# Optimization experiments

Hardware: AMD Instinct MI355X
Metric: run time of the kernel (lower is better)

## Reference

```python
import jax, jax.numpy as jnp
import numpy as np

B, T, H, ZS, ZT = 256, 512, 256, 64, 64
N_IRR = 2
TAU = 1.0
EPS = 1e-5

def setup_inputs() -> dict:
    key = jax.random.key(0)
    ks = jax.random.split(key, 32)
    def p(k, shape):
        return jax.random.normal(k, shape, jnp.float32) * 0.05
    gru_in_dim = ZT + H + 1 + N_IRR * 2  # 325
    return {
        "z_static": jax.random.normal(ks[0], (B, ZS), jnp.float32),
        "z_temporal": jax.random.normal(ks[1], (B, T, ZT), jnp.float32),
        "initial_states": jax.random.uniform(ks[2], (B, N_IRR, 2), jnp.float32),
        "sn_w1": p(ks[3], (H, ZS)), "sn_b1": p(ks[4], (H,)),
        "bn1_g": jnp.ones((H,), jnp.float32), "bn1_b": jnp.zeros((H,), jnp.float32),
        "sn_w2": p(ks[5], (H, H)), "sn_b2": p(ks[6], (H,)),
        "bn2_g": jnp.ones((H,), jnp.float32), "bn2_b": jnp.zeros((H,), jnp.float32),
        "sc_w": p(ks[7], (8, H)), "sc_b": p(ks[8], (8,)),
        "scat1_w": p(ks[9], (4, H)), "scat1_b": p(ks[10], (4,)),
        "scat2_w": p(ks[11], (6, H)), "scat2_b": p(ks[12], (6,)),
        "gru_wih": p(ks[13], (3 * H, gru_in_dim)), "gru_whh": p(ks[14], (3 * H, H)),
        "gru_bih": p(ks[15], (3 * H,)), "gru_bhh": p(ks[16], (3 * H,)),
        "tc_w": p(ks[17], (16, H)), "tc_b": p(ks[18], (16,)),
        "irr1_w": p(ks[19], (1, H)), "irr1_b": p(ks[20], (1,)),
        "irr2_w": p(ks[21], (1, H)), "irr2_b": p(ks[22], (1,)),
        "tcat_w": p(ks[23], (5, H)), "tcat_b": p(ks[24], (5,)),
    }

def _bn(x, g, b):
    # BatchNorm1d in training mode: batch stats, biased variance
    m = jnp.mean(x, axis=0)
    v = jnp.mean((x - m) ** 2, axis=0)
    return (x - m) * jax.lax.rsqrt(v + EPS) * g + b

def _gumbel_softmax(logits, k):
    g = jax.random.gumbel(k, logits.shape, logits.dtype)
    return jax.nn.softmax((logits + g) / TAU, axis=-1)

def _gru(x_proj, whh, bhh):
    # x_proj: [B,T,3H] = x @ Wih^T + bih, precomputed (big GEMM once)
    h0 = jnp.zeros((x_proj.shape[0], H), x_proj.dtype)
    def step(h, xp):
        gh = h @ whh.T + bhh
        xr, xz, xn = jnp.split(xp, 3, axis=-1)
        hr, hz, hn = jnp.split(gh, 3, axis=-1)
        r = jax.nn.sigmoid(xr + hr)
        z = jax.nn.sigmoid(xz + hz)
        n = jnp.tanh(xn + r * hn)
        h_new = (1.0 - z) * n + z * h
        return h_new, h_new
    _, hs = jax.lax.scan(step, h0, jnp.swapaxes(x_proj, 0, 1))  # [T,B,H]
    return jnp.swapaxes(hs, 0, 1)  # [B,T,H]

def _forward(z_static, z_temporal, initial_states, sn_w1, sn_b1, bn1_g, bn1_b,
             sn_w2, sn_b2, bn2_g, bn2_b, sc_w, sc_b, scat1_w, scat1_b,
             scat2_w, scat2_b, gru_wih, gru_whh, gru_bih, gru_bhh,
             tc_w, tc_b, irr1_w, irr1_b, irr2_w, irr2_b, tcat_w, tcat_b):
    b, t = z_temporal.shape[0], z_temporal.shape[1]
    baseline = _bn(jax.nn.relu(z_static @ sn_w1.T + sn_b1), bn1_g, bn1_b)
    baseline = _bn(jax.nn.relu(baseline @ sn_w2.T + sn_b2), bn2_g, bn2_b)  # [B,H]

    static_cont = jnp.tanh(baseline @ sc_w.T + sc_b) * 0.5 + 0.5  # [B,8]
    gk = jax.random.split(jax.random.key(42), 3)
    static_cat = jnp.concatenate([
        _gumbel_softmax(baseline @ scat1_w.T + scat1_b, gk[0]),
        _gumbel_softmax(baseline @ scat2_w.T + scat2_b, gk[1]),
    ], axis=-1)  # [B,10]

    baseline_exp = jnp.broadcast_to(baseline[:, None, :], (b, t, H))
    visit = jnp.broadcast_to(jnp.linspace(0.0, 1.0, t, dtype=z_temporal.dtype)[None, :, None], (b, t, 1))
    init = jnp.broadcast_to(initial_states.reshape(b, 1, N_IRR * 2), (b, t, N_IRR * 2))
    gru_in = jnp.concatenate([z_temporal, baseline_exp, visit, init], axis=-1)  # [B,T,325]

    x_proj = gru_in @ gru_wih.T + gru_bih  # [B,T,3H]
    h = _gru(x_proj, gru_whh, gru_bhh)  # [B,T,H]

    temporal_cont = jnp.tanh(h @ tc_w.T + tc_b) * 0.5 + 0.5  # [B,T,16]

    # irreversible hazards for the 2 binary vars, vectorized over vars: [B,T,2]
    hazard = jax.nn.sigmoid(jnp.concatenate([h @ irr1_w.T + irr1_b, h @ irr2_w.T + irr2_b], axis=-1))
    def irr_step(prev, hz_t):  # prev [B,N_IRR,2], hz_t [B,N_IRR]
        stay = prev[..., 1] > 0.5
        s1 = jnp.where(stay, 1.0, hz_t)
        s0 = jnp.where(stay, 0.0, 1.0 - hz_t)
        st = jnp.stack([s0, s1], axis=-1)
        return st, st
    _, tail = jax.lax.scan(irr_step, initial_states, jnp.swapaxes(hazard[:, 1:, :], 0, 1))
    states = jnp.concatenate([initial_states[:, None], jnp.moveaxis(tail, 0, 1)], axis=1)  # [B,T,N_IRR,2]

    tcat3 = _gumbel_softmax(h @ tcat_w.T + tcat_b, gk[2])  # [B,T,5]
    temporal_cat = jnp.concatenate([states[:, :, 0, :], states[:, :, 1, :], tcat3], axis=-1)  # [B,T,9]

    temporal_mask = jnp.ones((b, t, 1), h.dtype)
    return static_cont, static_cat, temporal_cont, temporal_cat, temporal_mask

def reference(z_static, z_temporal, initial_states, sn_w1, sn_b1, bn1_g, bn1_b,
              sn_w2, sn_b2, bn2_g, bn2_b, sc_w, sc_b, scat1_w, scat1_b,
              scat2_w, scat2_b, gru_wih, gru_whh, gru_bih, gru_bhh,
              tc_w, tc_b, irr1_w, irr1_b, irr2_w, irr2_b, tcat_w, tcat_b):
    return _forward(z_static, z_temporal, initial_states, sn_w1, sn_b1, bn1_g, bn1_b,
                    sn_w2, sn_b2, bn2_g, bn2_b, sc_w, sc_b, scat1_w, scat1_b,
                    scat2_w, scat2_b, gru_wih, gru_whh, gru_bih, gru_bhh,
                    tc_w, tc_b, irr1_w, irr1_b, irr2_w, irr2_b, tcat_w, tcat_b)
```

## Files before the change

### kernel.cpp

```cpp
#include <hip/hip_runtime.h>
#include <stdint.h>
#include <stddef.h>

#define NB 256
#define NT 512
#define NH 256
#define NZT 64
#define BN_EPS 1e-5f

#define OUT_SC    0
#define OUT_SCAT  2048
#define OUT_TC    4608
#define OUT_TCAT  2101760
#define OUT_MASK  3281408

#define WS_BL1    0
#define WS_BASE   65536
#define WS_BIAS   131072
#define WS_HHIST  327680
#define WS_HAZ    33882112
#define WS_BFRAG  34144256

typedef __bf16 bf16x8 __attribute__((ext_vector_type(8)));
typedef float f32x4v __attribute__((ext_vector_type(4)));

__host__ __device__ inline void tf2x32(uint32_t k0, uint32_t k1, uint32_t& x0, uint32_t& x1) {
  uint32_t k2 = k0 ^ k1 ^ 0x1BD11BDAu;
#define RR(d) { x0 += x1; x1 = (x1 << d) | (x1 >> (32 - d)); x1 ^= x0; }
  x0 += k0; x1 += k1;
  RR(13) RR(15) RR(26) RR(6)  x0 += k1; x1 += k2 + 1u;
  RR(17) RR(29) RR(16) RR(24) x0 += k2; x1 += k0 + 2u;
  RR(13) RR(15) RR(26) RR(6)  x0 += k0; x1 += k1 + 3u;
  RR(17) RR(29) RR(16) RR(24) x0 += k1; x1 += k2 + 4u;
  RR(13) RR(15) RR(26) RR(6)  x0 += k2; x1 += k0 + 5u;
#undef RR
}

__device__ inline float gumbel_pt(uint32_t k0, uint32_t k1, uint32_t idx) {
  uint32_t x0 = 0u, x1 = idx;
  tf2x32(k0, k1, x0, x1);
  uint32_t bits = x0 ^ x1;
  uint32_t fb = (bits >> 9) | 0x3F800000u;
  float f = __uint_as_float(fb) - 1.0f;
  const float TINY = 1.17549435e-38f;
  f = f * (1.0f - TINY) + TINY;
  f = fmaxf(TINY, f);
  return -logf(-logf(f));
}

__device__ inline uint16_t f2bf(float v) {
  uint32_t u = __float_as_uint(v);
  u += 0x7FFFu + ((u >> 16) & 1u);
  return (uint16_t)(u >> 16);
}
__device__ inline float bf2f(uint16_t h) { return __uint_as_float(((uint32_t)h) << 16); }

__device__ inline f32x4v mfma16(bf16x8 a, bf16x8 b, f32x4v c) {
  return __builtin_amdgcn_mfma_f32_16x16x32_bf16(a, b, c, 0, 0, 0);
}

__global__ void k_prep(const float* __restrict__ whh, const float* __restrict__ wih,
                       uint16_t* __restrict__ bfrag) {
  int gid = blockIdx.x * 256 + threadIdx.x;
  if (gid >= 61440) return;
  int l = gid & 63;
  int rest = gid >> 6;
  int part = rest & 1; rest >>= 1;
  int ks = rest % 10, ot = rest / 10;
  uint16_t outv[8];
#pragma unroll
  for (int j = 0; j < 8; ++j) {
    int k = ks * 32 + (l >> 4) * 8 + j;
    int o = ot * 16 + (l & 15);
    float v = (k < 256) ? whh[o * 256 + k] : wih[o * 325 + (k - 256)];
    uint16_t hi = f2bf(v);
    outv[j] = (part == 0) ? hi : f2bf(v - bf2f(hi));
  }
  *(uint4*)(bfrag + (size_t)gid * 8) = *(uint4*)outv;
}

__global__ void k_static(const float* __restrict__ x, int K, const float* __restrict__ w,
                         const float* __restrict__ bias, const float* __restrict__ g,
                         const float* __restrict__ bb, float* __restrict__ out) {
  int c = blockIdx.x, r = threadIdx.x;
  const float* wr = w + c * K;
  float acc = bias[c];
  for (int k = 0; k < K; ++k) acc += x[r * K + k] * wr[k];
  float v = fmaxf(acc, 0.0f);
  __shared__ float red[256];
  red[r] = v; __syncthreads();
  for (int s = 128; s > 0; s >>= 1) { if (r < s) red[r] += red[r + s]; __syncthreads(); }
  float m = red[0] * (1.0f / 256.0f);
  __syncthreads();
  float d = v - m;
  red[r] = d * d; __syncthreads();
  for (int s = 128; s > 0; s >>= 1) { if (r < s) red[r] += red[r + s]; __syncthreads(); }
  float var = red[0] * (1.0f / 256.0f);
  out[r * NH + c] = d * rsqrtf(var + BN_EPS) * g[c] + bb[c];
}

__global__ void k_bias(const float* __restrict__ baseline, const float* __restrict__ init,
                       const float* __restrict__ wih, const float* __restrict__ bih,
                       const float* __restrict__ bhh, float* __restrict__ bias2) {
  int b = blockIdx.x, tid = threadIdx.x;
  __shared__ float bl[256];
  __shared__ float in4[4];
  bl[tid] = baseline[b * 256 + tid];
  if (tid < 4) in4[tid] = init[b * 4 + tid];
  __syncthreads();
  for (int oo = 0; oo < 3; ++oo) {
    int o = oo * 256 + tid;
    const float* wr = wih + (size_t)o * 325;
    float acc = bih[o];
    for (int k = 0; k < 256; ++k) acc += bl[k] * wr[64 + k];
#pragma unroll
    for (int i = 0; i < 4; ++i) acc += in4[i] * wr[321 + i];
    if (o < 512) acc += bhh[o];
    bias2[b * 768 + o] = acc;
  }
}

__global__ void k_sheads(const float* __restrict__ baseline, const float* __restrict__ sc_w,
                         const float* __restrict__ sc_b, const float* __restrict__ s1w,
                         const float* __restrict__ s1b, const float* __restrict__ s2w,
                         const float* __restrict__ s2b, float* __restrict__ out,
                         uint32_t g0a, uint32_t g0b, uint32_t g1a, uint32_t g1b) {
  int b = blockIdx.x, tid = threadIdx.x;
  __shared__ float bl[256];
  __shared__ float lg[10];
  for (int i = tid; i < 256; i += 64) bl[i] = baseline[b * 256 + i];
  __syncthreads();
  if (tid < 18) {
    const float* wr; float bias;
    if (tid < 8)       { wr = sc_w + tid * 256;        bias = sc_b[tid]; }
    else if (tid < 12) { wr = s1w + (tid - 8) * 256;   bias = s1b[tid - 8]; }
    else               { wr = s2w + (tid - 12) * 256;  bias = s2b[tid - 12]; }
    float acc = bias;
    for (int k = 0; k < 256; ++k) acc += bl[k] * wr[k];
    if (tid < 8)       out[OUT_SC + b * 8 + tid] = tanhf(acc) * 0.5f + 0.5f;
    else if (tid < 12) lg[tid - 8] = acc + gumbel_pt(g0a, g0b, (uint32_t)(b * 4 + (tid - 8)));
    else               lg[tid - 8] = acc + gumbel_pt(g1a, g1b, (uint32_t)(b * 6 + (tid - 12)));
  }
  __syncthreads();
  if (tid == 0) {
    float m = fmaxf(fmaxf(lg[0], lg[1]), fmaxf(lg[2], lg[3]));
    float e[4], s = 0.f;
    for (int i = 0; i < 4; ++i) { e[i] = expf(lg[i] - m); s += e[i]; }
    float* o1 = out + OUT_SCAT + b * 10;
    for (int i = 0; i < 4; ++i) o1[i] = e[i] / s;
  } else if (tid == 1) {
    float m = lg[4];
    for (int i = 5; i < 10; ++i) m = fmaxf(m, lg[i]);
    float e[6], s = 0.f;
    for (int i = 0; i < 6; ++i) { e[i] = expf(lg[4 + i] - m); s += e[i]; }
    float* o1 = out + OUT_SCAT + b * 10 + 4;
    for (int i = 0; i < 6; ++i) o1[i] = e[i] / s;
  }
}

__global__ __launch_bounds__(256, 1)
void k_persist(const float* __restrict__ zt, const uint16_t* __restrict__ bfrag,
               const float* __restrict__ bias2, const float* __restrict__ wih,
               const float* __restrict__ bhh, float* __restrict__ h_hist) {
  int bb = blockIdx.x;
  int tid = threadIdx.x;
  int w = tid >> 6, lane = tid & 63;
  int l15 = lane & 15, l4 = lane >> 4;

  __shared__ __align__(16) uint16_t afr[10][2][64][8];
  __shared__ __align__(16) float hbuf[16][260];

  for (int i = tid; i < 16 * 260; i += 256) ((float*)hbuf)[i] = 0.0f;

  bf16x8 Brg[2][12][2];
#pragma unroll
  for (int oti = 0; oti < 12; ++oti) {
    int ot = (oti >> 2) * 16 + w * 4 + (oti & 3);
    const uint16_t* p = bfrag + (size_t)ot * 10240 + lane * 8;
    Brg[0][oti][0] = *(const bf16x8*)(p);
    Brg[0][oti][1] = *(const bf16x8*)(p + 512);
    Brg[1][oti][0] = *(const bf16x8*)(p + 1024);
    Brg[1][oti][1] = *(const bf16x8*)(p + 1536);
  }

  float b2r[4][4], b2z[4][4], b2x[4][4], bhn4[4], wvr[4], wvz[4], wvn[4];
#pragma unroll
  for (int q = 0; q < 4; ++q) {
    int j = (w * 4 + q) * 16 + l15;
    wvr[q] = wih[(size_t)j * 325 + 320];
    wvz[q] = wih[(size_t)(256 + j) * 325 + 320];
    wvn[q] = wih[(size_t)(512 + j) * 325 + 320];
    bhn4[q] = bhh[512 + j];
#pragma unroll
    for (int r = 0; r < 4; ++r) {
      int brow = bb * 16 + l4 * 4 + r;
      b2r[q][r] = bias2[brow * 768 + j];
      b2z[q][r] = bias2[brow * 768 + 256 + j];
      b2x[q][r] = bias2[brow * 768 + 512 + j];
    }
  }

  const float* zbase = zt + (size_t)(bb * 16 + (tid >> 4)) * NT * NZT + (tid & 15) * 4;
  float4 zv = *(const float4*)zbase;

  const uint16_t* baseB = bfrag + (size_t)lane * 8;

  __syncthreads();

#pragma unroll 1
  for (int t = 0; t < NT; ++t) {
#pragma unroll
    for (int i = 0; i < 2; ++i) {
      int it = tid + i * 256;
      int b = it >> 5, k8 = it & 31;
      float4 v0 = *(const float4*)&hbuf[b][k8 * 8];
      float4 v1 = *(const float4*)&hbuf[b][k8 * 8 + 4];
      float v[8] = {v0.x, v0.y, v0.z, v0.w, v1.x, v1.y, v1.z, v1.w};
      uint16_t hi[8], lo[8];
#pragma unroll
      for (int j = 0; j < 8; ++j) { hi[j] = f2bf(v[j]); lo[j] = f2bf(v[j] - bf2f(hi[j])); }
      int lz = b + ((k8 & 3) << 4);
      *(uint4*)&afr[k8 >> 2][0][lz][0] = *(uint4*)hi;
      *(uint4*)&afr[k8 >> 2][1][lz][0] = *(uint4*)lo;
    }
    {
      int b = tid >> 4, kq = tid & 15;
      float zarr[4] = {zv.x, zv.y, zv.z, zv.w};
      uint16_t hi[4], lo[4];
#pragma unroll
      for (int j = 0; j < 4; ++j) { hi[j] = f2bf(zarr[j]); lo[j] = f2bf(zarr[j] - bf2f(hi[j])); }
      int ks = 8 + (kq >> 3);
      int lz = b + (((kq & 7) >> 1) << 4);
      int e0 = (kq & 1) * 4;
      *(uint2*)&afr[ks][0][lz][e0] = *(uint2*)hi;
      *(uint2*)&afr[ks][1][lz][e0] = *(uint2*)lo;
    }
    float4 znext = zv;
    if (t + 1 < NT) znext = *(const float4*)(zbase + (size_t)(t + 1) * NZT);
    __syncthreads();

    f32x4v accs[4][4];
#pragma unroll
    for (int q = 0; q < 4; ++q)
#pragma unroll
      for (int g = 0; g < 4; ++g) accs[q][g] = (f32x4v){0.f, 0.f, 0.f, 0.f};

#pragma unroll
    for (int ks = 0; ks < 10; ++ks) {
      bf16x8 Ah = *(const bf16x8*)&afr[ks][0][lane][0];
      bf16x8 Al = *(const bf16x8*)&afr[ks][1][lane][0];
#pragma unroll
      for (int g = 0; g < 3; ++g) {
        const int gi = (g < 2) ? g : ((ks < 8) ? 2 : 3);
        bf16x8 bh[4], bl[4];
#pragma unroll
        for (int q = 0; q < 4; ++q) {
          const int oti = g * 4 + q;
          if (ks < 2) {
            bh[q] = Brg[ks][oti][0];
            bl[q] = Brg[ks][oti][1];
          } else {
            int ot = g * 16 + w * 4 + q;
            const uint16_t* p = baseB + (size_t)ot * 10240 + ks * 1024;
            bh[q] = *(const bf16x8*)(p);
            bl[q] = *(const bf16x8*)(p + 512);
          }
        }
#pragma unroll
        for (int q = 0; q < 4; ++q) accs[q][gi] = mfma16(Ah, bh[q], accs[q][gi]);
#pragma unroll
        for (int q = 0; q < 4; ++q) accs[q][gi] = mfma16(Ah, bl[q], accs[q][gi]);
#pragma unroll
        for (int q = 0; q < 4; ++q) accs[q][gi] = mfma16(Al, bh[q], accs[q][gi]);
      }
    }

    float visit = (float)t * (1.0f / 511.0f);
#pragma unroll
    for (int q = 0; q < 4; ++q) {
      int jcol = (w * 4 + q) * 16 + l15;
#pragma unroll
      for (int r = 0; r < 4; ++r) {
        int m = l4 * 4 + r;
        float lr = accs[q][0][r] + b2r[q][r] + visit * wvr[q];
        float lz = accs[q][1][r] + b2z[q][r] + visit * wvz[q];
        float hn = accs[q][2][r] + bhn4[q];
        float xn = accs[q][3][r] + b2x[q][r] + visit * wvn[q];
        float rg = 1.0f / (1.0f + __expf(-lr));
        float zg = 1.0f / (1.0f + __expf(-lz));
        float e2 = __expf(2.0f * (xn + rg * hn));
        float ng = 1.0f - 2.0f / (e2 + 1.0f);
        float hp = hbuf[m][jcol];
        float hv = (1.0f - zg) * ng + zg * hp;
        hbuf[m][jcol] = hv;
        h_hist[((size_t)(bb * 16 + m) * NT + t) * NH + jcol] = hv;
      }
    }
    __syncthreads();
    zv = znext;
  }
}

__global__ __launch_bounds__(256)
void k_heads(const float* __restrict__ h_hist, const float* __restrict__ tcw,
             const float* __restrict__ tcb, const float* __restrict__ i1w,
             const float* __restrict__ i1b, const float* __restrict__ i2w,
             const float* __restrict__ i2b, const float* __restrict__ tcatw,
             const float* __restrict__ tcatb, float* __restrict__ out,
             float* __restrict__ hazard, uint32_t g2a, uint32_t g2b) {
  int r = blockIdx.x * 256 + threadIdx.x;
  const float* hr = h_hist + (size_t)r * 256;
  float a[16] = {0.f}; float ai0 = 0.f, ai1 = 0.f; float at[5] = {0.f};
  for (int k4 = 0; k4 < 64; ++k4) {
    float4 hv = *(const float4*)(hr + k4 * 4);
#pragma unroll
    for (int i = 0; i < 16; ++i) {
      float4 wv = *(const float4*)(tcw + i * 256 + k4 * 4);
      a[i] += hv.x * wv.x + hv.y * wv.y + hv.z * wv.z + hv.w * wv.w;
    }
    { float4 wv = *(const float4*)(i1w + k4 * 4); ai0 += hv.x * wv.x + hv.y * wv.y + hv.z * wv.z + hv.w * wv.w; }
    { float4 wv = *(const float4*)(i2w + k4 * 4); ai1 += hv.x * wv.x + hv.y * wv.y + hv.z * wv.z + hv.w * wv.w; }
#pragma unroll
    for (int i = 0; i < 5; ++i) {
      float4 wv = *(const float4*)(tcatw + i * 256 + k4 * 4);
      at[i] += hv.x * wv.x + hv.y * wv.y + hv.z * wv.z + hv.w * wv.w;
    }
  }
  float* o2 = out + OUT_TC + (size_t)r * 16;
#pragma unroll
  for (int i = 0; i < 16; ++i) o2[i] = tanhf(a[i] + tcb[i]) * 0.5f + 0.5f;
  float h0 = 1.0f / (1.0f + expf(-(ai0 + i1b[0])));
  float h1 = 1.0f / (1.0f + expf(-(ai1 + i2b[0])));
  hazard[(size_t)r * 2 + 0] = h0;
  hazard[(size_t)r * 2 + 1] = h1;
  float lg[5];
#pragma unroll
  for (int i = 0; i < 5; ++i) lg[i] = at[i] + tcatb[i] + gumbel_pt(g2a, g2b, (uint32_t)(r * 5 + i));
  float m = lg[0];
#pragma unroll
  for (int i = 1; i < 5; ++i) m = fmaxf(m, lg[i]);
  float e[5], s = 0.f;
#pragma unroll
  for (int i = 0; i < 5; ++i) { e[i] = expf(lg[i] - m); s += e[i]; }
  float* o3 = out + OUT_TCAT + (size_t)r * 9;
#pragma unroll
  for (int i = 0; i < 5; ++i) o3[4 + i] = e[i] / s;
  out[OUT_MASK + r] = 1.0f;
}

__global__ void k_scan(const float* __restrict__ init, const float* __restrict__ hazard,
                       float* __restrict__ out) {
  int w = threadIdx.x >> 6, l = threadIdx.x & 63;
  int task = blockIdx.x * 4 + w;
  int b = task >> 1, var = task & 1;
  float hz[8]; int tmin = 1 << 20;
#pragma unroll
  for (int c = 0; c < 8; ++c) {
    int t = 1 + c * 64 + l;
    hz[c] = 0.0f;
    if (t < NT) {
      hz[c] = hazard[((size_t)b * NT + t) * 2 + var];
      if (hz[c] > 0.5f) tmin = min(tmin, t);
    }
  }
#pragma unroll
  for (int m = 32; m > 0; m >>= 1) tmin = min(tmin, __shfl_xor(tmin, m));
  float s1i = init[b * 4 + var * 2 + 1];
  if (s1i > 0.5f) tmin = 0;
  float* tc = out + OUT_TCAT + (size_t)b * NT * 9 + var * 2;
  if (l == 0) { tc[0] = init[b * 4 + var * 2]; tc[1] = s1i; }
#pragma unroll
  for (int c = 0; c < 8; ++c) {
    int t = 1 + c * 64 + l;
    if (t < NT) {
      bool ab = t > tmin;
      float s1 = ab ? 1.0f : hz[c];
      float s0 = ab ? 0.0f : 1.0f - hz[c];
      tc[(size_t)t * 9 + 0] = s0;
      tc[(size_t)t * 9 + 1] = s1;
    }
  }
}

extern "C" void kernel_launch(void* const* d_in, const int* in_sizes, int n_in,
                              void* d_out, int out_size, void* d_ws, size_t ws_size,
                              hipStream_t stream) {
  (void)in_sizes; (void)n_in; (void)out_size; (void)ws_size;
  const float* z_static = (const float*)d_in[0];
  const float* z_temporal = (const float*)d_in[1];
  const float* initial_states = (const float*)d_in[2];
  const float* sn_w1 = (const float*)d_in[3];
  const float* sn_b1 = (const float*)d_in[4];
  const float* bn1_g = (const float*)d_in[5];
  const float* bn1_b = (const float*)d_in[6];
  const float* sn_w2 = (const float*)d_in[7];
  const float* sn_b2 = (const float*)d_in[8];
  const float* bn2_g = (const float*)d_in[9];
  const float* bn2_b = (const float*)d_in[10];
  const float* sc_w = (const float*)d_in[11];
  const float* sc_b = (const float*)d_in[12];
  const float* scat1_w = (const float*)d_in[13];
  const float* scat1_b = (const float*)d_in[14];
  const float* scat2_w = (const float*)d_in[15];
  const float* scat2_b = (const float*)d_in[16];
  const float* gru_wih = (const float*)d_in[17];
  const float* gru_whh = (const float*)d_in[18];
  const float* gru_bih = (const float*)d_in[19];
  const float* gru_bhh = (const float*)d_in[20];
  const float* tc_w = (const float*)d_in[21];
  const float* tc_b = (const float*)d_in[22];
  const float* irr1_w = (const float*)d_in[23];
  const float* irr1_b = (const float*)d_in[24];
  const float* irr2_w = (const float*)d_in[25];
  const float* irr2_b = (const float*)d_in[26];
  const float* tcat_w = (const float*)d_in[27];
  const float* tcat_b = (const float*)d_in[28];

  float* out = (float*)d_out;
  float* ws = (float*)d_ws;
  float* bl1 = ws + WS_BL1;
  float* baseline = ws + WS_BASE;
  float* bias2 = ws + WS_BIAS;
  float* h_hist = ws + WS_HHIST;
  float* hazard = ws + WS_HAZ;
  uint16_t* bfrag = (uint16_t*)(ws + WS_BFRAG);

  uint32_t gk[3][2];
  for (uint32_t i = 0; i < 3; ++i) {
    uint32_t a = 0u, b = i;
    tf2x32(0u, 42u, a, b);
    gk[i][0] = a; gk[i][1] = b;
  }

  k_prep<<<240, 256, 0, stream>>>(gru_whh, gru_wih, bfrag);
  k_static<<<256, 256, 0, stream>>>(z_static, 64, sn_w1, sn_b1, bn1_g, bn1_b, bl1);
  k_static<<<256, 256, 0, stream>>>(bl1, 256, sn_w2, sn_b2, bn2_g, bn2_b, baseline);
  k_bias<<<256, 256, 0, stream>>>(baseline, initial_states, gru_wih, gru_bih, gru_bhh, bias2);
  k_sheads<<<256, 64, 0, stream>>>(baseline, sc_w, sc_b, scat1_w, scat1_b, scat2_w, scat2_b,
                                   out, gk[0][0], gk[0][1], gk[1][0], gk[1][1]);

  k_persist<<<16, 256, 0, stream>>>(z_temporal, bfrag, bias2, gru_wih, gru_bhh, h_hist);

  k_heads<<<512, 256, 0, stream>>>(h_hist, tc_w, tc_b, irr1_w, irr1_b, irr2_w, irr2_b,
                                   tcat_w, tcat_b, out, hazard, gk[2][0], gk[2][1]);
  k_scan<<<128, 256, 0, stream>>>(initial_states, hazard, out);
}
```

Measured before the change: 13.37 ms.

## Double waves in persistent GRU kernel and software-pipeline B-fragment loads

```diff
diff --git a/kernel.cpp b/kernel.cpp
--- a/kernel.cpp
+++ b/kernel.cpp
@@ -158,7 +158,7 @@
   }
 }
 
-__global__ __launch_bounds__(256, 1)
+__global__ __launch_bounds__(512, 2)
 void k_persist(const float* __restrict__ zt, const uint16_t* __restrict__ bfrag,
                const float* __restrict__ bias2, const float* __restrict__ wih,
                const float* __restrict__ bhh, float* __restrict__ h_hist) {
@@ -166,53 +166,44 @@
   int tid = threadIdx.x;
   int w = tid >> 6, lane = tid & 63;
   int l15 = lane & 15, l4 = lane >> 4;
+  int q0 = w * 2;
 
   __shared__ __align__(16) uint16_t afr[10][2][64][8];
   __shared__ __align__(16) float hbuf[16][260];
 
-  for (int i = tid; i < 16 * 260; i += 256) ((float*)hbuf)[i] = 0.0f;
-
-  bf16x8 Brg[2][12][2];
-#pragma unroll
-  for (int oti = 0; oti < 12; ++oti) {
-    int ot = (oti >> 2) * 16 + w * 4 + (oti & 3);
-    const uint16_t* p = bfrag + (size_t)ot * 10240 + lane * 8;
-    Brg[0][oti][0] = *(const bf16x8*)(p);
-    Brg[0][oti][1] = *(const bf16x8*)(p + 512);
-    Brg[1][oti][0] = *(const bf16x8*)(p + 1024);
-    Brg[1][oti][1] = *(const bf16x8*)(p + 1536);
-  }
-
-  float b2r[4][4], b2z[4][4], b2x[4][4], bhn4[4], wvr[4], wvz[4], wvn[4];
-#pragma unroll
-  for (int q = 0; q < 4; ++q) {
-    int j = (w * 4 + q) * 16 + l15;
-    wvr[q] = wih[(size_t)j * 325 + 320];
-    wvz[q] = wih[(size_t)(256 + j) * 325 + 320];
-    wvn[q] = wih[(size_t)(512 + j) * 325 + 320];
-    bhn4[q] = bhh[512 + j];
+  for (int i = tid; i < 16 * 260; i += 512) ((float*)hbuf)[i] = 0.0f;
+
+  float b2r[2][4], b2z[2][4], b2x[2][4], bhn2[2], wvr[2], wvz[2], wvn[2];
+#pragma unroll
+  for (int qq = 0; qq < 2; ++qq) {
+    int j = (q0 + qq) * 16 + l15;
+    wvr[qq] = wih[(size_t)j * 325 + 320];
+    wvz[qq] = wih[(size_t)(256 + j) * 325 + 320];
+    wvn[qq] = wih[(size_t)(512 + j) * 325 + 320];
+    bhn2[qq] = bhh[512 + j];
 #pragma unroll
     for (int r = 0; r < 4; ++r) {
       int brow = bb * 16 + l4 * 4 + r;
-      b2r[q][r] = bias2[brow * 768 + j];
-      b2z[q][r] = bias2[brow * 768 + 256 + j];
-      b2x[q][r] = bias2[brow * 768 + 512 + j];
-    }
-  }
-
-  const float* zbase = zt + (size_t)(bb * 16 + (tid >> 4)) * NT * NZT + (tid & 15) * 4;
-  float4 zv = *(const float4*)zbase;
+      b2r[qq][r] = bias2[brow * 768 + j];
+      b2z[qq][r] = bias2[brow * 768 + 256 + j];
+      b2x[qq][r] = bias2[brow * 768 + 512 + j];
+    }
+  }
+
+  const float* zbase = zt + (size_t)(bb * 16 + ((tid & 255) >> 4)) * NT * NZT + (tid & 15) * 4;
+  float4 zv = {0.f, 0.f, 0.f, 0.f};
+  if (tid < 256) zv = *(const float4*)zbase;
 
   const uint16_t* baseB = bfrag + (size_t)lane * 8;
+#define BADDR(ks, g, qq, part) ((const bf16x8*)(baseB + \
+    ((size_t)((g) * 16 + q0 + (qq)) * 10240 + (ks) * 1024 + (part) * 512)))
 
   __syncthreads();
 
 #pragma unroll 1
   for (int t = 0; t < NT; ++t) {
-#pragma unroll
-    for (int i = 0; i < 2; ++i) {
-      int it = tid + i * 256;
-      int b = it >> 5, k8 = it & 31;
+    {
+      int b = tid >> 5, k8 = tid & 31;
       float4 v0 = *(const float4*)&hbuf[b][k8 * 8];
       float4 v1 = *(const float4*)&hbuf[b][k8 * 8 + 4];
       float v[8] = {v0.x, v0.y, v0.z, v0.w, v1.x, v1.y, v1.z, v1.w};
@@ -223,7 +214,7 @@
       *(uint4*)&afr[k8 >> 2][0][lz][0] = *(uint4*)hi;
       *(uint4*)&afr[k8 >> 2][1][lz][0] = *(uint4*)lo;
     }
-    {
+    if (tid < 256) {
       int b = tid >> 4, kq = tid & 15;
       float zarr[4] = {zv.x, zv.y, zv.z, zv.w};
       uint16_t hi[4], lo[4];
@@ -236,56 +227,64 @@
       *(uint2*)&afr[ks][1][lz][e0] = *(uint2*)lo;
     }
     float4 znext = zv;
-    if (t + 1 < NT) znext = *(const float4*)(zbase + (size_t)(t + 1) * NZT);
+    if (tid < 256 && t + 1 < NT) znext = *(const float4*)(zbase + (size_t)(t + 1) * NZT);
     __syncthreads();
 
-    f32x4v accs[4][4];
-#pragma unroll
-    for (int q = 0; q < 4; ++q)
-#pragma unroll
-      for (int g = 0; g < 4; ++g) accs[q][g] = (f32x4v){0.f, 0.f, 0.f, 0.f};
-
-#pragma unroll
-    for (int ks = 0; ks < 10; ++ks) {
-      bf16x8 Ah = *(const bf16x8*)&afr[ks][0][lane][0];
-      bf16x8 Al = *(const bf16x8*)&afr[ks][1][lane][0];
-#pragma unroll
-      for (int g = 0; g < 3; ++g) {
-        const int gi = (g < 2) ? g : ((ks < 8) ? 2 : 3);
-        bf16x8 bh[4], bl[4];
-#pragma unroll
-        for (int q = 0; q < 4; ++q) {
-          const int oti = g * 4 + q;
-          if (ks < 2) {
-            bh[q] = Brg[ks][oti][0];
-            bl[q] = Brg[ks][oti][1];
-          } else {
-            int ot = g * 16 + w * 4 + q;
-            const uint16_t* p = baseB + (size_t)ot * 10240 + ks * 1024;
-            bh[q] = *(const bf16x8*)(p);
-            bl[q] = *(const bf16x8*)(p + 512);
-          }
-        }
-#pragma unroll
-        for (int q = 0; q < 4; ++q) accs[q][gi] = mfma16(Ah, bh[q], accs[q][gi]);
-#pragma unroll
-        for (int q = 0; q < 4; ++q) accs[q][gi] = mfma16(Ah, bl[q], accs[q][gi]);
-#pragma unroll
-        for (int q = 0; q < 4; ++q) accs[q][gi] = mfma16(Al, bh[q], accs[q][gi]);
+    f32x4v accs[2][4];
+#pragma unroll
+    for (int qq = 0; qq < 2; ++qq)
+#pragma unroll
+      for (int g = 0; g < 4; ++g) accs[qq][g] = (f32x4v){0.f, 0.f, 0.f, 0.f};
+
+    bf16x8 A2h[2], A2l[2];
+    A2h[0] = *(const bf16x8*)&afr[0][0][lane][0];
+    A2l[0] = *(const bf16x8*)&afr[0][1][lane][0];
+
+    bf16x8 bq[4][4];
+#pragma unroll
+    for (int s = 0; s < 3; ++s) {
+      bq[s][0] = *BADDR(0, s, 0, 0);
+      bq[s][1] = *BADDR(0, s, 0, 1);
+      bq[s][2] = *BADDR(0, s, 1, 0);
+      bq[s][3] = *BADDR(0, s, 1, 1);
+    }
+
+#pragma unroll
+    for (int s = 0; s < 30; ++s) {
+      const int ks = s / 3, g = s % 3;
+      const int gi = (g < 2) ? g : ((ks < 8) ? 2 : 3);
+      if (g == 0 && ks < 9) {
+        A2h[(ks + 1) & 1] = *(const bf16x8*)&afr[ks + 1][0][lane][0];
+        A2l[(ks + 1) & 1] = *(const bf16x8*)&afr[ks + 1][1][lane][0];
       }
+      if (s + 3 < 30) {
+        const int ks2 = (s + 3) / 3, g2 = (s + 3) % 3, sl = (s + 3) & 3;
+        bq[sl][0] = *BADDR(ks2, g2, 0, 0);
+        bq[sl][1] = *BADDR(ks2, g2, 0, 1);
+        bq[sl][2] = *BADDR(ks2, g2, 1, 0);
+        bq[sl][3] = *BADDR(ks2, g2, 1, 1);
+      }
+      bf16x8 Ah = A2h[ks & 1], Al = A2l[ks & 1];
+      const int sl0 = s & 3;
+      accs[0][gi] = mfma16(Ah, bq[sl0][0], accs[0][gi]);
+      accs[1][gi] = mfma16(Ah, bq[sl0][2], accs[1][gi]);
+      accs[0][gi] = mfma16(Ah, bq[sl0][1], accs[0][gi]);
+      accs[1][gi] = mfma16(Ah, bq[sl0][3], accs[1][gi]);
+      accs[0][gi] = mfma16(Al, bq[sl0][0], accs[0][gi]);
+      accs[1][gi] = mfma16(Al, bq[sl0][2], accs[1][gi]);
     }
 
     float visit = (float)t * (1.0f / 511.0f);
 #pragma unroll
-    for (int q = 0; q < 4; ++q) {
-      int jcol = (w * 4 + q) * 16 + l15;
+    for (int qq = 0; qq < 2; ++qq) {
+      int jcol = (q0 + qq) * 16 + l15;
 #pragma unroll
       for (int r = 0; r < 4; ++r) {
         int m = l4 * 4 + r;
-        float lr = accs[q][0][r] + b2r[q][r] + visit * wvr[q];
-        float lz = accs[q][1][r] + b2z[q][r] + visit * wvz[q];
-        float hn = accs[q][2][r] + bhn4[q];
-        float xn = accs[q][3][r] + b2x[q][r] + visit * wvn[q];
+        float lr = accs[qq][0][r] + b2r[qq][r] + visit * wvr[qq];
+        float lz = accs[qq][1][r] + b2z[qq][r] + visit * wvz[qq];
+        float hn = accs[qq][2][r] + bhn2[qq];
+        float xn = accs[qq][3][r] + b2x[qq][r] + visit * wvn[qq];
         float rg = 1.0f / (1.0f + __expf(-lr));
         float zg = 1.0f / (1.0f + __expf(-lz));
         float e2 = __expf(2.0f * (xn + rg * hn));
@@ -299,6 +298,7 @@
     __syncthreads();
     zv = znext;
   }
+#undef BADDR
 }
 
 __global__ __launch_bounds__(256)
@@ -439,7 +439,7 @@
   k_sheads<<<256, 64, 0, stream>>>(baseline, sc_w, sc_b, scat1_w, scat1_b, scat2_w, scat2_b,
                                    out, gk[0][0], gk[0][1], gk[1][0], gk[1][1]);
 
-  k_persist<<<16, 256, 0, stream>>>(z_temporal, bfrag, bias2, gru_wih, gru_bhh, h_hist);
+  k_persist<<<16, 512, 0, stream>>>(z_temporal, bfrag, bias2, gru_wih, gru_bhh, h_hist);
 
   k_heads<<<512, 256, 0, stream>>>(h_hist, tc_w, tc_b, irr1_w, irr1_b, irr2_w, irr2_b,
                                    tcat_w, tcat_b, out, hazard, gk[2][0], gk[2][1]);
```

Result: faster. 10.97 ms (-18.0%).
